# Kernel optimization log

Hardware: AMD Instinct MI355X
Metric: run time of the kernel (lower is better)

The kernel has to match this reference:

```python
import jax, jax.numpy as jnp
import numpy as np

EMBED = 1024
HEADS = 16
HEAD_DIM = EMBED // HEADS
HIDDEN = 4 * EMBED
EPS = 1e-5


def setup_inputs() -> dict:
    key = jax.random.key(0)
    ks = jax.random.split(key, 9)
    s = lambda fan_in: 1.0 / np.sqrt(fan_in)
    inp = {
        "x": jax.random.normal(ks[0], (2, 2048, EMBED), dtype=jnp.float32),
        "ln1_w": jnp.ones((EMBED,), jnp.float32),
        "ln1_b": jnp.zeros((EMBED,), jnp.float32),
        "ln2_w": jnp.ones((EMBED,), jnp.float32),
        "ln2_b": jnp.zeros((EMBED,), jnp.float32),
        "qkv_w": jax.random.uniform(ks[1], (EMBED, 3 * EMBED), jnp.float32, -s(EMBED), s(EMBED)),
        "qkv_b": jax.random.uniform(ks[2], (3 * EMBED,), jnp.float32, -s(EMBED), s(EMBED)),
        "proj_w": jax.random.uniform(ks[3], (EMBED, EMBED), jnp.float32, -s(EMBED), s(EMBED)),
        "proj_b": jax.random.uniform(ks[4], (EMBED,), jnp.float32, -s(EMBED), s(EMBED)),
        "fc1_w": jax.random.uniform(ks[5], (EMBED, HIDDEN), jnp.float32, -s(EMBED), s(EMBED)),
        "fc1_b": jax.random.uniform(ks[6], (HIDDEN,), jnp.float32, -s(EMBED), s(EMBED)),
        "fc2_w": jax.random.uniform(ks[7], (HIDDEN, EMBED), jnp.float32, -s(HIDDEN), s(HIDDEN)),
        "fc2_b": jax.random.uniform(ks[8], (EMBED,), jnp.float32, -s(HIDDEN), s(HIDDEN)),
    }
    return inp


def _layernorm(x, w, b):
    mu = jnp.mean(x, axis=-1, keepdims=True)
    var = jnp.mean(jnp.square(x - mu), axis=-1, keepdims=True)
    return (x - mu) * jax.lax.rsqrt(var + EPS) * w + b


def _attn(x, qkv_w, qkv_b, proj_w, proj_b):
    B, N, C = x.shape
    qkv = x @ qkv_w + qkv_b                      # [B,N,3C]
    qkv = qkv.reshape(B, N, 3, HEADS, HEAD_DIM)
    q, k, v = qkv[:, :, 0], qkv[:, :, 1], qkv[:, :, 2]   # [B,N,H,D]
    scale = HEAD_DIM ** -0.5
    scores = jnp.einsum("bqhd,bkhd->bhqk", q, k) * scale  # [B,H,N,N]
    attn = jax.nn.softmax(scores, axis=-1)
    out = jnp.einsum("bhqk,bkhd->bqhd", attn, v).reshape(B, N, C)
    return out @ proj_w + proj_b


def _mlp(x, fc1_w, fc1_b, fc2_w, fc2_b):
    h = jax.nn.gelu(x @ fc1_w + fc1_b, approximate=False)
    return h @ fc2_w + fc2_b


def reference(x, ln1_w, ln1_b, ln2_w, ln2_b, qkv_w, qkv_b, proj_w, proj_b,
              fc1_w, fc1_b, fc2_w, fc2_b):
    # pre-norm transformer block (eval mode: dropout/drop_path are identity)
    x = x + _attn(_layernorm(x, ln1_w, ln1_b), qkv_w, qkv_b, proj_w, proj_b)
    x = x + _mlp(_layernorm(x, ln2_w, ln2_b), fc1_w, fc1_b, fc2_w, fc2_b)
    return x
```

## Files before the change

### kernel.cpp

```cpp
#include <hip/hip_runtime.h>
#include <hip/hip_bf16.h>

#define SEQ    2048
#define BATCH  2
#define MTOK   4096
#define EMBED  1024
#define HEADS  16
#define HDIM   64
#define QKV3   3072
#define FFN    4096

typedef __attribute__((ext_vector_type(8))) short bf16x8;
typedef __attribute__((ext_vector_type(4))) float f32x4;
typedef __attribute__((ext_vector_type(16))) float f32x16;

static __device__ __forceinline__ unsigned short f2bf(float f) {
  union { float f; unsigned u; } x; x.f = f;
  unsigned r = x.u + 0x7FFFu + ((x.u >> 16) & 1u);
  return (unsigned short)(r >> 16);
}
static __device__ __forceinline__ float bf2f(unsigned short u) {
  union { unsigned u; float f; } x; x.u = ((unsigned)u) << 16; return x.f;
}
static __device__ __forceinline__ unsigned pk2bf(float a, float b) {
#if __has_builtin(__builtin_amdgcn_cvt_pk_bf16_f32)
  typedef __attribute__((ext_vector_type(2))) __bf16 bf16x2_t;
  union { bf16x2_t v; unsigned u; } x;
  x.v = __builtin_amdgcn_cvt_pk_bf16_f32(a, b);
  return x.u;
#else
  return ((unsigned)f2bf(a)) | (((unsigned)f2bf(b)) << 16);
#endif
}
static __device__ __forceinline__ float fexp2(float x) {
#if __has_builtin(__builtin_amdgcn_exp2f)
  return __builtin_amdgcn_exp2f(x);
#else
  return exp2f(x);
#endif
}
static __device__ __forceinline__ float frcp(float x) {
#if __has_builtin(__builtin_amdgcn_rcpf)
  return __builtin_amdgcn_rcpf(x);
#else
  return 1.0f / x;
#endif
}
static __device__ __forceinline__ float fgelu(float v) {
  float t = v * v;
  float z = v * __builtin_fmaf(-0.1029456f, t, -2.3022650687f);
  return v * frcp(1.0f + fexp2(z));
}

static __device__ __forceinline__ void halfswap(unsigned a, unsigned b, int hi,
                                                unsigned& lo_out, unsigned& hi_out) {
#if __has_builtin(__builtin_amdgcn_permlane32_swap)
  typedef __attribute__((ext_vector_type(2))) unsigned uint2v;
  uint2v r = __builtin_amdgcn_permlane32_swap(a, b, false, false);
  lo_out = r[0];
  hi_out = r[1];
#else
  unsigned as = (unsigned)__shfl_xor((int)a, 32);
  unsigned bs = (unsigned)__shfl_xor((int)b, 32);
  lo_out = hi ? bs : a;
  hi_out = hi ? b : as;
#endif
}

static __device__ __forceinline__ void gload16(const unsigned short* g, unsigned short* l) {
  __builtin_amdgcn_global_load_lds((const __attribute__((address_space(1))) void*)g,
                                   (__attribute__((address_space(3))) void*)l, 16, 0, 0);
}

#define MEMFENCE asm volatile("" ::: "memory")

struct TD { const float* W; unsigned short* T; int K, N, ntx, base; };
struct TD4 { TD d[4]; };

__global__ void transpose_all(TD4 td) {
  __shared__ float t[32][33];
  int bid = blockIdx.x;
  int i = 0;
  if (bid >= td.d[1].base) i = 1;
  if (bid >= td.d[2].base) i = 2;
  if (bid >= td.d[3].base) i = 3;
  const TD& D = td.d[i];
  int local = bid - D.base;
  int n0 = (local % D.ntx) * 32, k0 = (local / D.ntx) * 32;
  int tx = threadIdx.x, ty = threadIdx.y;
#pragma unroll
  for (int j = 0; j < 32; j += 8)
    t[ty + j][tx] = D.W[(size_t)(k0 + ty + j) * D.N + n0 + tx];
  __syncthreads();
#pragma unroll
  for (int j = 0; j < 32; j += 8)
    D.T[(size_t)(n0 + ty + j) * D.K + k0 + tx] = f2bf(t[tx][ty + j]);
}

__global__ __launch_bounds__(256) void ln_kernel(const float* __restrict__ in,
                                                 const float* __restrict__ w,
                                                 const float* __restrict__ b,
                                                 unsigned short* __restrict__ out) {
  __shared__ float sh[4];
  int row = blockIdx.x, tid = threadIdx.x;
  const float4 v = ((const float4*)(in + (size_t)row * EMBED))[tid];
  float s = v.x + v.y + v.z + v.w;
#pragma unroll
  for (int off = 32; off; off >>= 1) s += __shfl_xor(s, off);
  if ((tid & 63) == 0) sh[tid >> 6] = s;
  __syncthreads();
  float mean = (sh[0] + sh[1] + sh[2] + sh[3]) * (1.0f / EMBED);
  __syncthreads();
  float dx = v.x - mean, dy = v.y - mean, dz = v.z - mean, dw = v.w - mean;
  float q = dx * dx + dy * dy + dz * dz + dw * dw;
#pragma unroll
  for (int off = 32; off; off >>= 1) q += __shfl_xor(q, off);
  if ((tid & 63) == 0) sh[tid >> 6] = q;
  __syncthreads();
  float var = (sh[0] + sh[1] + sh[2] + sh[3]) * (1.0f / EMBED);
  float rs = rsqrtf(var + 1e-5f);
  const float4 wv = ((const float4*)w)[tid];
  const float4 bv = ((const float4*)b)[tid];
  ushort4 o;
  o.x = f2bf(dx * rs * wv.x + bv.x);
  o.y = f2bf(dy * rs * wv.y + bv.y);
  o.z = f2bf(dz * rs * wv.z + bv.z);
  o.w = f2bf(dw * rs * wv.w + bv.w);
  ((ushort4*)(out + (size_t)row * EMBED))[tid] = o;
}

template <int ACT, int OUTBF, int VSPLIT>
__global__ __launch_bounds__(256) void gemmBig(const unsigned short* __restrict__ A,
                                               const unsigned short* __restrict__ Wt,
                                               const float* __restrict__ bias,
                                               unsigned short* __restrict__ outB,
                                               float* __restrict__ outF,
                                               unsigned short* __restrict__ vT,
                                               int M, int N, int K, int nblk) {
  __shared__ __align__(16) unsigned short As[128 * 64];
  __shared__ __align__(16) unsigned short Bs[128 * 64];
  const int tid = threadIdx.x;
  const int wave = tid >> 6, lane = tid & 63;
  const int quad = lane >> 4, ml = lane & 15;
  const int wr = wave >> 1, wc = wave & 1;
  const int m0 = (blockIdx.x / nblk) * 128;
  const int n0 = (blockIdx.x % nblk) * 128;
  const int srow = lane >> 3;
  const int schunk = (lane & 7) ^ (srow & 7);
  const unsigned short* Ag = A + (size_t)(m0 + wave * 32 + srow) * K + schunk * 8;
  const unsigned short* Bg = Wt + (size_t)(n0 + wave * 32 + srow) * K + schunk * 8;
  unsigned short* AsW = &As[wave * 2048];
  unsigned short* BsW = &Bs[wave * 2048];
  f32x4 acc[4][4];
#pragma unroll
  for (int i = 0; i < 4; i++)
#pragma unroll
    for (int j = 0; j < 4; j++) acc[i][j] = (f32x4){0.f, 0.f, 0.f, 0.f};
  for (int k0 = 0; k0 < K; k0 += 64) {
    __syncthreads();
#pragma unroll
    for (int t = 0; t < 4; t++) {
      gload16(Ag + (size_t)(8 * t) * K, AsW + 512 * t);
      gload16(Bg + (size_t)(8 * t) * K, BsW + 512 * t);
    }
    Ag += 64; Bg += 64;
    __syncthreads();
#pragma unroll
    for (int kh = 0; kh < 2; kh++) {
      const int ch = ((kh * 4 + quad) ^ (ml & 7)) * 8;
      bf16x8 af[4], bfr[4];
#pragma unroll
      for (int mt = 0; mt < 4; mt++)
        af[mt] = *(const bf16x8*)&As[(wr * 64 + mt * 16 + ml) * 64 + ch];
#pragma unroll
      for (int nt = 0; nt < 4; nt++)
        bfr[nt] = *(const bf16x8*)&Bs[(wc * 64 + nt * 16 + ml) * 64 + ch];
#pragma unroll
      for (int mt = 0; mt < 4; mt++)
#pragma unroll
        for (int nt = 0; nt < 4; nt++)
          acc[mt][nt] = __builtin_amdgcn_mfma_f32_16x16x32_bf16(af[mt], bfr[nt], acc[mt][nt], 0, 0, 0);
    }
  }
#pragma unroll
  for (int mt = 0; mt < 4; mt++)
#pragma unroll
    for (int nt = 0; nt < 4; nt++) {
      const int col0 = n0 + wc * 64 + nt * 16;
      const int row0 = m0 + wr * 64 + mt * 16;
      if (VSPLIT && col0 >= 2 * EMBED) {
        const int b = row0 >> 11, tok0 = row0 & (SEQ - 1);
        const int h = (col0 - 2 * EMBED) >> 6;
        const int dl = ((col0 - 2 * EMBED) & 63) + ml;
        float bia = bias[col0 + ml];
        ushort4 o;
        o.x = f2bf(acc[mt][nt][0] + bia);
        o.y = f2bf(acc[mt][nt][1] + bia);
        o.z = f2bf(acc[mt][nt][2] + bia);
        o.w = f2bf(acc[mt][nt][3] + bia);
        *(ushort4*)(vT + (size_t)((b * 16 + h) * 64 + dl) * SEQ + tok0 + quad * 4) = o;
      } else {
#pragma unroll
        for (int r = 0; r < 4; r++) {
          int row = row0 + quad * 4 + r;
          int col = col0 + ml;
          float v = acc[mt][nt][r] + bias[col];
          if (ACT) v = fgelu(v);
          if (OUTBF)
            outB[(size_t)row * N + col] = f2bf(v);
          else
            outF[(size_t)row * N + col] = v;
        }
      }
    }
}

template <int ACT, int VSPLIT>
__global__ __launch_bounds__(512, 2) void gemm256(const unsigned short* __restrict__ A,
                                                  const unsigned short* __restrict__ Wt,
                                                  const float* __restrict__ bias,
                                                  unsigned short* __restrict__ outB,
                                                  unsigned short* __restrict__ vT,
                                                  int M, int N, int K, int nblk) {
  __shared__ __align__(16) unsigned short As[2][256 * 64];
  __shared__ __align__(16) unsigned short Bs[2][256 * 64];
  const int tid = threadIdx.x;
  const int wave = tid >> 6, lane = tid & 63;
  const int quad = lane >> 4, ml = lane & 15;
  const int wr = wave >> 2, wc = wave & 3;
  const int m0 = (blockIdx.x / nblk) * 256;
  const int n0 = (blockIdx.x % nblk) * 256;
  const int srow = lane >> 3;
  const int schunk = (lane & 7) ^ (srow & 7);
  const unsigned short* Ag = A  + (size_t)(m0 + wave * 32 + srow) * K + schunk * 8;
  const unsigned short* Bg = Wt + (size_t)(n0 + wave * 32 + srow) * K + schunk * 8;
  f32x4 acc[8][4];
#pragma unroll
  for (int i = 0; i < 8; i++)
#pragma unroll
    for (int j = 0; j < 4; j++) acc[i][j] = (f32x4){0.f, 0.f, 0.f, 0.f};

#pragma unroll
  for (int g = 0; g < 4; g++) {
    gload16(Ag + (size_t)(g * 8) * K, &As[0][(wave * 32 + g * 8) * 64]);
    gload16(Bg + (size_t)(g * 8) * K, &Bs[0][(wave * 32 + g * 8) * 64]);
  }

  const int nit = K >> 7;
  for (int it = 0; it < nit; ++it) {
#pragma unroll
    for (int half = 0; half < 2; ++half) {
      const int rs = half;
      const int ss = half ^ 1;
      const int kst = 2 * it + 1 + half;
      const bool doStage = (kst < 2 * nit);
      const unsigned short* Asl = &As[rs][0];
      const unsigned short* Bsl = &Bs[rs][0];
      bf16x8 bfr[4][2];
#pragma unroll
      for (int ph = 0; ph < 4; ++ph) {
        bf16x8 af[2][2];
        if (ph > 0) {
#pragma unroll
          for (int mt2 = 0; mt2 < 2; ++mt2)
#pragma unroll
            for (int kk = 0; kk < 2; ++kk)
              af[mt2][kk] = *(const bf16x8*)&Asl[(wr * 128 + (ph * 2 + mt2) * 16 + ml) * 64 +
                                                ((kk * 4 + quad) ^ (ml & 7)) * 8];
        }
        if (doStage) {
          if (ph < 2) {
            gload16(Ag + (size_t)((ph * 2) * 8) * K + kst * 64,
                    &As[ss][(wave * 32 + (ph * 2) * 8) * 64]);
            gload16(Ag + (size_t)((ph * 2 + 1) * 8) * K + kst * 64,
                    &As[ss][(wave * 32 + (ph * 2 + 1) * 8) * 64]);
          } else {
            gload16(Bg + (size_t)(((ph - 2) * 2) * 8) * K + kst * 64,
                    &Bs[ss][(wave * 32 + ((ph - 2) * 2) * 8) * 64]);
            gload16(Bg + (size_t)(((ph - 2) * 2 + 1) * 8) * K + kst * 64,
                    &Bs[ss][(wave * 32 + ((ph - 2) * 2 + 1) * 8) * 64]);
          }
        }
        if (ph == 0) {
          if (doStage) { asm volatile("s_waitcnt vmcnt(2)" ::: "memory"); }
          else         { asm volatile("s_waitcnt vmcnt(0)" ::: "memory"); }
          MEMFENCE; __builtin_amdgcn_s_barrier(); MEMFENCE;
#pragma unroll
          for (int nt = 0; nt < 4; ++nt)
#pragma unroll
            for (int kk = 0; kk < 2; ++kk)
              bfr[nt][kk] = *(const bf16x8*)&Bsl[(wc * 64 + nt * 16 + ml) * 64 +
                                                ((kk * 4 + quad) ^ (ml & 7)) * 8];
#pragma unroll
          for (int mt2 = 0; mt2 < 2; ++mt2)
#pragma unroll
            for (int kk = 0; kk < 2; ++kk)
              af[mt2][kk] = *(const bf16x8*)&Asl[(wr * 128 + mt2 * 16 + ml) * 64 +
                                                ((kk * 4 + quad) ^ (ml & 7)) * 8];
        } else {
          MEMFENCE; __builtin_amdgcn_s_barrier(); MEMFENCE;
        }
        __builtin_amdgcn_s_setprio(1);
#pragma unroll
        for (int mt2 = 0; mt2 < 2; ++mt2)
#pragma unroll
          for (int nt = 0; nt < 4; ++nt)
#pragma unroll
            for (int kk = 0; kk < 2; ++kk)
              acc[ph * 2 + mt2][nt] = __builtin_amdgcn_mfma_f32_16x16x32_bf16(
                  af[mt2][kk], bfr[nt][kk], acc[ph * 2 + mt2][nt], 0, 0, 0);
        __builtin_amdgcn_s_setprio(0);
        MEMFENCE; __builtin_amdgcn_s_barrier(); MEMFENCE;
      }
    }
  }
#pragma unroll
  for (int mt = 0; mt < 8; ++mt)
#pragma unroll
    for (int nt = 0; nt < 4; ++nt) {
      const int col0 = n0 + wc * 64 + nt * 16;
      const int row0 = m0 + wr * 128 + mt * 16;
      if (VSPLIT && col0 >= 2 * EMBED) {
        const int b = row0 >> 11, tok0 = row0 & (SEQ - 1);
        const int h = (col0 - 2 * EMBED) >> 6;
        const int dl = ((col0 - 2 * EMBED) & 63) + ml;
        float bia = bias[col0 + ml];
        ushort4 o;
        o.x = f2bf(acc[mt][nt][0] + bia);
        o.y = f2bf(acc[mt][nt][1] + bia);
        o.z = f2bf(acc[mt][nt][2] + bia);
        o.w = f2bf(acc[mt][nt][3] + bia);
        *(ushort4*)(vT + (size_t)((b * 16 + h) * 64 + dl) * SEQ + tok0 + quad * 4) = o;
      } else {
#pragma unroll
        for (int r = 0; r < 4; ++r) {
          int row = row0 + quad * 4 + r;
          int col = col0 + ml;
          float v = acc[mt][nt][r] + bias[col];
          if (ACT) v = fgelu(v);
          outB[(size_t)row * N + col] = f2bf(v);
        }
      }
    }
}

template <int RES, int OUTBF>
__global__ __launch_bounds__(256) void gemm64k(const unsigned short* __restrict__ A,
                                               const unsigned short* __restrict__ Wt,
                                               const float* __restrict__ bias,
                                               const float* __restrict__ res,
                                               unsigned short* __restrict__ outB,
                                               float* __restrict__ outF,
                                               int M, int N, int K, int nblk) {
  __shared__ __align__(16) unsigned short As[3][128 * 64];
  __shared__ __align__(16) unsigned short Bs[3][64 * 64];
  const int tid = threadIdx.x;
  const int wave = tid >> 6, lane = tid & 63;
  const int quad = lane >> 4, ml = lane & 15;
  const int wr = wave >> 1, wc = wave & 1;
  const int xcd = blockIdx.x & 7, idx = blockIdx.x >> 3;
  const int mPerXcd = (gridDim.x >> 3) / nblk;
  const int m0 = (xcd * mPerXcd + idx / nblk) * 128;
  const int n0 = (idx % nblk) * 64;
  const int srow = lane >> 3;
  const int schunk = (lane & 7) ^ (srow & 7);
  const unsigned short* Ag = A + (size_t)(m0 + wave * 32 + srow) * K + schunk * 8;
  const unsigned short* Bg = Wt + (size_t)(n0 + wave * 16 + srow) * K + schunk * 8;
  f32x4 acc[4][2];
#pragma unroll
  for (int i = 0; i < 4; i++) { acc[i][0] = (f32x4){0.f,0.f,0.f,0.f}; acc[i][1] = acc[i][0]; }

#pragma unroll
  for (int p = 0; p < 2; ++p) {
    unsigned short* AsW = &As[p][wave * 2048];
    unsigned short* BsW = &Bs[p][wave * 1024];
    gload16(Ag, AsW);
    gload16(Ag + (size_t)8 * K,  AsW + 512);
    gload16(Ag + (size_t)16 * K, AsW + 1024);
    gload16(Ag + (size_t)24 * K, AsW + 1536);
    gload16(Bg, BsW);
    gload16(Bg + (size_t)8 * K,  BsW + 512);
    Ag += 64; Bg += 64;
  }

  const int nk = K >> 6;
  int ss = 2;
  for (int kk = 0; kk < nk; ++kk) {
    if (kk + 2 < nk) {
      unsigned short* AsW = &As[ss][wave * 2048];
      unsigned short* BsW = &Bs[ss][wave * 1024];
      gload16(Ag, AsW);
      gload16(Ag + (size_t)8 * K,  AsW + 512);
      gload16(Ag + (size_t)16 * K, AsW + 1024);
      gload16(Ag + (size_t)24 * K, AsW + 1536);
      gload16(Bg, BsW);
      gload16(Bg + (size_t)8 * K,  BsW + 512);
      Ag += 64; Bg += 64;
      asm volatile("s_waitcnt vmcnt(12)" ::: "memory");
    } else if (kk + 1 < nk) {
      asm volatile("s_waitcnt vmcnt(6)" ::: "memory");
    } else {
      asm volatile("s_waitcnt vmcnt(0)" ::: "memory");
    }
    MEMFENCE; __builtin_amdgcn_s_barrier(); MEMFENCE;
    const int cs = kk - 3 * ((kk * 0x5556) >> 16);
    const unsigned short* Asl = &As[cs][0];
    const unsigned short* Bsl = &Bs[cs][0];
#pragma unroll
    for (int kh = 0; kh < 2; kh++) {
      const int ch = ((kh * 4 + quad) ^ (ml & 7)) * 8;
      bf16x8 af[4], bfr[2];
#pragma unroll
      for (int mt = 0; mt < 4; mt++)
        af[mt] = *(const bf16x8*)&Asl[(wr * 64 + mt * 16 + ml) * 64 + ch];
#pragma unroll
      for (int nt = 0; nt < 2; nt++)
        bfr[nt] = *(const bf16x8*)&Bsl[(wc * 32 + nt * 16 + ml) * 64 + ch];
#pragma unroll
      for (int mt = 0; mt < 4; mt++)
#pragma unroll
        for (int nt = 0; nt < 2; nt++)
          acc[mt][nt] = __builtin_amdgcn_mfma_f32_16x16x32_bf16(af[mt], bfr[nt], acc[mt][nt], 0, 0, 0);
    }
    MEMFENCE; __builtin_amdgcn_s_barrier(); MEMFENCE;
    ss = (ss == 2) ? 0 : ss + 1;
  }
#pragma unroll
  for (int mt = 0; mt < 4; mt++)
#pragma unroll
    for (int nt = 0; nt < 2; nt++)
#pragma unroll
      for (int r = 0; r < 4; r++) {
        int row = m0 + wr * 64 + mt * 16 + quad * 4 + r;
        int col = n0 + wc * 32 + nt * 16 + ml;
        float v = acc[mt][nt][r] + bias[col];
        if (RES) v += res[(size_t)row * N + col];
        if (OUTBF)
          outB[(size_t)row * N + col] = f2bf(v);
        else
          outF[(size_t)row * N + col] = v;
      }
}

__global__ __launch_bounds__(256, 4) void attn_kernel(const unsigned short* __restrict__ qkv,
                                                      const unsigned short* __restrict__ vT,
                                                      unsigned short* __restrict__ attn) {
  __shared__ __align__(16) unsigned short Ks[2][64 * 64];
  __shared__ __align__(16) unsigned short Vs[2][64 * 64];
  const int tid = threadIdx.x, wave = tid >> 6, lane = tid & 63;
  const int l31 = lane & 31, hi = lane >> 5;
  const int qs = wave & 1, kh = wave >> 1;
  const int bh = blockIdx.x, b = bh >> 4, h = bh & 15;
  const int q0w = blockIdx.y * 64 + qs * 32;
  const float qscale = 0.18033688011112042f;
  const int sw = l31 & 7;

  const unsigned short* qrow = qkv + (size_t)(b * SEQ + q0w + l31) * QKV3 + h * HDIM;
  bf16x8 bq[4];
#pragma unroll
  for (int s = 0; s < 4; s++) {
    bq[s] = *(const bf16x8*)(qrow + s * 16 + hi * 8);
#pragma unroll
    for (int j = 0; j < 8; j++)
      bq[s][j] = (short)f2bf(bf2f((unsigned short)bq[s][j]) * qscale);
  }
  bf16x8 ones;
#pragma unroll
  for (int j = 0; j < 8; j++) ones[j] = (short)0x3F80;

  f32x16 zz;
#pragma unroll
  for (int i = 0; i < 16; i++) zz[i] = 0.f;
  f32x16 O0 = zz, O1 = zz, lsum = zz;

  const int skey = lane >> 3;
  const int schunk8 = ((lane & 7) ^ (skey & 7)) * 8;
  const unsigned short* kbase =
      qkv + (size_t)(b * SEQ + wave * 16 + skey) * QKV3 + EMBED + h * HDIM + schunk8;
  const unsigned short* vbase =
      vT + (size_t)(bh * 64 + wave * 16 + skey) * SEQ + schunk8;

  gload16(kbase, &Ks[0][wave * 1024]);
  gload16(kbase + (size_t)8 * QKV3, &Ks[0][wave * 1024] + 512);
  gload16(vbase, &Vs[0][wave * 1024]);
  gload16(vbase + (size_t)8 * SEQ, &Vs[0][wave * 1024] + 512);
  __syncthreads();

  const int krow0 = kh * 32;
  for (int kti = 0; kti < SEQ / 64; ++kti) {
    const int cur = kti & 1;
    if (kti + 1 < SEQ / 64) {
      const int kt = (kti + 1) * 64;
      unsigned short* kd = &Ks[cur ^ 1][wave * 1024];
      unsigned short* vd = &Vs[cur ^ 1][wave * 1024];
      gload16(kbase + (size_t)kt * QKV3, kd);
      gload16(kbase + (size_t)(kt + 8) * QKV3, kd + 512);
      gload16(vbase + kt, vd);
      gload16(vbase + kt + (size_t)8 * SEQ, vd + 512);
    }
    const unsigned short* Kc = &Ks[cur][0];
    const unsigned short* Vc = &Vs[cur][0];

    f32x16 St = zz;
#pragma unroll
    for (int s = 0; s < 4; s++) {
      bf16x8 ak = *(const bf16x8*)&Kc[(krow0 + l31) * 64 + ((2 * s + hi) ^ sw) * 8];
      St = __builtin_amdgcn_mfma_f32_32x32x16_bf16(ak, bq[s], St, 0, 0, 0);
    }

    unsigned W0[4], W1[4];
#pragma unroll
    for (int g = 0; g < 4; g++) {
      W0[g] = pk2bf(fexp2(St[4 * g]), fexp2(St[4 * g + 1]));
      W1[g] = pk2bf(fexp2(St[4 * g + 2]), fexp2(St[4 * g + 3]));
    }

    bf16x8 pa[2];
#pragma unroll
    for (int ks = 0; ks < 2; ks++) {
      const int g0 = 2 * ks, g1 = g0 + 1;
      unsigned w0, w1, w2, w3;
      halfswap(W0[g0], W0[g1], hi, w0, w2);
      halfswap(W1[g0], W1[g1], hi, w1, w3);
      union { unsigned u[4]; bf16x8 v; } pw;
      pw.u[0] = w0; pw.u[1] = w1; pw.u[2] = w2; pw.u[3] = w3;
      pa[ks] = pw.v;
    }

    __builtin_amdgcn_s_setprio(1);
    lsum = __builtin_amdgcn_mfma_f32_32x32x16_bf16(pa[0], ones, lsum, 0, 0, 0);
    lsum = __builtin_amdgcn_mfma_f32_32x32x16_bf16(pa[1], ones, lsum, 0, 0, 0);
#pragma unroll
    for (int ks = 0; ks < 2; ks++) {
      const int ch = kh * 4 + ks * 2 + hi;
      bf16x8 bv0 = *(const bf16x8*)&Vc[l31 * 64 + (ch ^ sw) * 8];
      bf16x8 bv1 = *(const bf16x8*)&Vc[(32 + l31) * 64 + (ch ^ sw) * 8];
      O0 = __builtin_amdgcn_mfma_f32_32x32x16_bf16(pa[ks], bv0, O0, 0, 0, 0);
      O1 = __builtin_amdgcn_mfma_f32_32x32x16_bf16(pa[ks], bv1, O1, 0, 0, 0);
    }
    __builtin_amdgcn_s_setprio(0);
    __syncthreads();
  }

  if (kh == 1) {
    float* sc = qs ? (float*)&Vs[0][0] : (float*)&Ks[0][0];
#pragma unroll
    for (int r = 0; r < 16; r++) {
      sc[lane * 49 + r]      = lsum[r];
      sc[lane * 49 + 16 + r] = O0[r];
      sc[lane * 49 + 32 + r] = O1[r];
    }
  }
  __syncthreads();
  if (kh == 0) {
    const float* sc = qs ? (const float*)&Vs[0][0] : (const float*)&Ks[0][0];
#pragma unroll
    for (int r = 0; r < 16; r++) {
      lsum[r] += sc[lane * 49 + r];
      O0[r]   += sc[lane * 49 + 16 + r];
      O1[r]   += sc[lane * 49 + 32 + r];
    }
#pragma unroll
    for (int r = 0; r < 16; r++) {
      const int qr = (r & 3) + 8 * (r >> 2) + 4 * hi;
      float inv = 1.0f / lsum[r];
      size_t g = (size_t)(b * SEQ + q0w + qr) * EMBED + h * HDIM + l31;
      attn[g]      = f2bf(O0[r] * inv);
      attn[g + 32] = f2bf(O1[r] * inv);
    }
  }
}

extern "C" void kernel_launch(void* const* d_in, const int* in_sizes, int n_in,
                              void* d_out, int out_size, void* d_ws, size_t ws_size,
                              hipStream_t stream) {
  const float* x      = (const float*)d_in[0];
  const float* ln1_w  = (const float*)d_in[1];
  const float* ln1_b  = (const float*)d_in[2];
  const float* ln2_w  = (const float*)d_in[3];
  const float* ln2_b  = (const float*)d_in[4];
  const float* qkv_w  = (const float*)d_in[5];
  const float* qkv_b  = (const float*)d_in[6];
  const float* proj_w = (const float*)d_in[7];
  const float* proj_b = (const float*)d_in[8];
  const float* fc1_w  = (const float*)d_in[9];
  const float* fc1_b  = (const float*)d_in[10];
  const float* fc2_w  = (const float*)d_in[11];
  const float* fc2_b  = (const float*)d_in[12];
  float* out = (float*)d_out;
  char* wsb = (char*)d_ws;
  unsigned short* lnbuf  = (unsigned short*)(wsb + 0);
  unsigned short* qkvb   = (unsigned short*)(wsb + 8388608);
  unsigned short* attnb  = (unsigned short*)(wsb + 33554432);
  unsigned short* vTb    = (unsigned short*)(wsb + 41943040);
  unsigned short* actb   = (unsigned short*)(wsb + 33554432);
  float*          h1     = (float*)(wsb + 67108864);
  unsigned short* qkvWt  = (unsigned short*)(wsb + 83886080);
  unsigned short* projWt = (unsigned short*)(wsb + 90177536);
  unsigned short* fc1Wt  = (unsigned short*)(wsb + 92274688);
  unsigned short* fc2Wt  = (unsigned short*)(wsb + 100663296);

  TD4 td;
  td.d[0] = {qkv_w,  qkvWt,  1024, 3072,  96, 0};
  td.d[1] = {proj_w, projWt, 1024, 1024,  32, 3072};
  td.d[2] = {fc1_w,  fc1Wt,  1024, 4096, 128, 4096};
  td.d[3] = {fc2_w,  fc2Wt,  4096, 1024,  32, 8192};
  transpose_all<<<12288, dim3(32, 8), 0, stream>>>(td);

  ln_kernel<<<MTOK, 256, 0, stream>>>(x, ln1_w, ln1_b, lnbuf);
  gemmBig<0, 1, 1><<<768, 256, 0, stream>>>(
      lnbuf, qkvWt, qkv_b, qkvb, nullptr, vTb, MTOK, QKV3, EMBED, 24);
  attn_kernel<<<dim3(32, 32), 256, 0, stream>>>(qkvb, vTb, attnb);
  gemm64k<1, 0><<<512, 256, 0, stream>>>(
      attnb, projWt, proj_b, x, nullptr, h1, MTOK, EMBED, EMBED, 16);
  ln_kernel<<<MTOK, 256, 0, stream>>>(h1, ln2_w, ln2_b, lnbuf);
  gemm256<1, 0><<<256, 512, 0, stream>>>(
      lnbuf, fc1Wt, fc1_b, actb, nullptr, MTOK, FFN, EMBED, 16);
  gemm64k<1, 0><<<512, 256, 0, stream>>>(
      actb, fc2Wt, fc2_b, h1, nullptr, out, MTOK, EMBED, FFN, 16);
}
```

Baseline: 337.9 us.

## Double attention block to 8 waves with 128-key tiles and four-way key split

The attention kernel moves from 256 to 512 threads. Each block now stages 128-key K/V tiles per iteration with a new 16-way XOR swizzle for the V tile, so half as many loop iterations and barriers are needed. The key dimension is split across four wave groups instead of two, and partial softmax sums and outputs are combined in a two-stage shared-memory reduction. Shared memory per block doubles and extra barriers are added at the end, which may limit occupancy under the 512x4 launch bound.

Result: no change. 340.0 us (+0.6%).

```diff
diff --git a/kernel.cpp b/kernel.cpp
--- a/kernel.cpp
+++ b/kernel.cpp
@@ -442,11 +442,11 @@
       }
 }
 
-__global__ __launch_bounds__(256, 4) void attn_kernel(const unsigned short* __restrict__ qkv,
+__global__ __launch_bounds__(512, 4) void attn_kernel(const unsigned short* __restrict__ qkv,
                                                       const unsigned short* __restrict__ vT,
                                                       unsigned short* __restrict__ attn) {
-  __shared__ __align__(16) unsigned short Ks[2][64 * 64];
-  __shared__ __align__(16) unsigned short Vs[2][64 * 64];
+  __shared__ __align__(16) unsigned short Ks[2][128 * 64];
+  __shared__ __align__(16) unsigned short Vs[2][64 * 128];
   const int tid = threadIdx.x, wave = tid >> 6, lane = tid & 63;
   const int l31 = lane & 31, hi = lane >> 5;
   const int qs = wave & 1, kh = wave >> 1;
@@ -477,26 +477,28 @@
   const int schunk8 = ((lane & 7) ^ (skey & 7)) * 8;
   const unsigned short* kbase =
       qkv + (size_t)(b * SEQ + wave * 16 + skey) * QKV3 + EMBED + h * HDIM + schunk8;
-  const unsigned short* vbase =
-      vT + (size_t)(bh * 64 + wave * 16 + skey) * SEQ + schunk8;
+  const int vr0 = wave * 8 + (lane >> 4);
+  const int vr1 = vr0 + 4;
+  const unsigned short* vbase0 =
+      vT + (size_t)(bh * 64 + vr0) * SEQ + (((lane & 15) ^ (vr0 & 15)) * 8);
+  const unsigned short* vbase1 =
+      vT + (size_t)(bh * 64 + vr1) * SEQ + (((lane & 15) ^ (vr1 & 15)) * 8);
 
   gload16(kbase, &Ks[0][wave * 1024]);
   gload16(kbase + (size_t)8 * QKV3, &Ks[0][wave * 1024] + 512);
-  gload16(vbase, &Vs[0][wave * 1024]);
-  gload16(vbase + (size_t)8 * SEQ, &Vs[0][wave * 1024] + 512);
+  gload16(vbase0, &Vs[0][wave * 1024]);
+  gload16(vbase1, &Vs[0][wave * 1024 + 512]);
   __syncthreads();
 
   const int krow0 = kh * 32;
-  for (int kti = 0; kti < SEQ / 64; ++kti) {
+  for (int kti = 0; kti < SEQ / 128; ++kti) {
     const int cur = kti & 1;
-    if (kti + 1 < SEQ / 64) {
-      const int kt = (kti + 1) * 64;
-      unsigned short* kd = &Ks[cur ^ 1][wave * 1024];
-      unsigned short* vd = &Vs[cur ^ 1][wave * 1024];
-      gload16(kbase + (size_t)kt * QKV3, kd);
-      gload16(kbase + (size_t)(kt + 8) * QKV3, kd + 512);
-      gload16(vbase + kt, vd);
-      gload16(vbase + kt + (size_t)8 * SEQ, vd + 512);
+    if (kti + 1 < SEQ / 128) {
+      const int kt = (kti + 1) * 128;
+      gload16(kbase + (size_t)kt * QKV3, &Ks[cur ^ 1][wave * 1024]);
+      gload16(kbase + (size_t)(kt + 8) * QKV3, &Ks[cur ^ 1][wave * 1024] + 512);
+      gload16(vbase0 + kt, &Vs[cur ^ 1][wave * 1024]);
+      gload16(vbase1 + kt, &Vs[cur ^ 1][wave * 1024 + 512]);
     }
     const unsigned short* Kc = &Ks[cur][0];
     const unsigned short* Vc = &Vs[cur][0];
@@ -533,8 +535,8 @@
 #pragma unroll
     for (int ks = 0; ks < 2; ks++) {
       const int ch = kh * 4 + ks * 2 + hi;
-      bf16x8 bv0 = *(const bf16x8*)&Vc[l31 * 64 + (ch ^ sw) * 8];
-      bf16x8 bv1 = *(const bf16x8*)&Vc[(32 + l31) * 64 + (ch ^ sw) * 8];
+      bf16x8 bv0 = *(const bf16x8*)&Vc[l31 * 128 + ((ch ^ (l31 & 15))) * 8];
+      bf16x8 bv1 = *(const bf16x8*)&Vc[(32 + l31) * 128 + ((ch ^ (l31 & 15))) * 8];
       O0 = __builtin_amdgcn_mfma_f32_32x32x16_bf16(pa[ks], bv0, O0, 0, 0, 0);
       O1 = __builtin_amdgcn_mfma_f32_32x32x16_bf16(pa[ks], bv1, O1, 0, 0, 0);
     }
@@ -542,8 +544,10 @@
     __syncthreads();
   }
 
-  if (kh == 1) {
-    float* sc = qs ? (float*)&Vs[0][0] : (float*)&Ks[0][0];
+  float* A2 = qs ? (float*)&Vs[0][0] : (float*)&Ks[0][0];
+  float* A3 = qs ? (float*)&Vs[1][0] : (float*)&Ks[1][0];
+  if (kh == 2 || kh == 3) {
+    float* sc = (kh == 2) ? A2 : A3;
 #pragma unroll
     for (int r = 0; r < 16; r++) {
       sc[lane * 49 + r]      = lsum[r];
@@ -552,13 +556,31 @@
     }
   }
   __syncthreads();
-  if (kh == 0) {
-    const float* sc = qs ? (const float*)&Vs[0][0] : (const float*)&Ks[0][0];
+  if (kh == 0 || kh == 1) {
+    const float* sc = (kh == 0) ? A2 : A3;
 #pragma unroll
     for (int r = 0; r < 16; r++) {
       lsum[r] += sc[lane * 49 + r];
       O0[r]   += sc[lane * 49 + 16 + r];
       O1[r]   += sc[lane * 49 + 32 + r];
+    }
+  }
+  __syncthreads();
+  if (kh == 1) {
+#pragma unroll
+    for (int r = 0; r < 16; r++) {
+      A2[lane * 49 + r]      = lsum[r];
+      A2[lane * 49 + 16 + r] = O0[r];
+      A2[lane * 49 + 32 + r] = O1[r];
+    }
+  }
+  __syncthreads();
+  if (kh == 0) {
+#pragma unroll
+    for (int r = 0; r < 16; r++) {
+      lsum[r] += A2[lane * 49 + r];
+      O0[r]   += A2[lane * 49 + 16 + r];
+      O1[r]   += A2[lane * 49 + 32 + r];
     }
 #pragma unroll
     for (int r = 0; r < 16; r++) {
@@ -610,7 +632,7 @@
   ln_kernel<<<MTOK, 256, 0, stream>>>(x, ln1_w, ln1_b, lnbuf);
   gemmBig<0, 1, 1><<<768, 256, 0, stream>>>(
       lnbuf, qkvWt, qkv_b, qkvb, nullptr, vTb, MTOK, QKV3, EMBED, 24);
-  attn_kernel<<<dim3(32, 32), 256, 0, stream>>>(qkvb, vTb, attnb);
+  attn_kernel<<<dim3(32, 32), 512, 0, stream>>>(qkvb, vTb, attnb);
   gemm64k<1, 0><<<512, 256, 0, stream>>>(
       attnb, projWt, proj_b, x, nullptr, h1, MTOK, EMBED, EMBED, 16);
   ln_kernel<<<MTOK, 256, 0, stream>>>(h1, ln2_w, ln2_b, lnbuf);
```

## Split-K the fc2 GEMM into two halves with a separate reduce kernel

Applied to the files above, without the earlier changes.

The fc2 GEMM (K=4096) now launches 1024 blocks, each computing half of the K range and writing fp32 partial sums to a workspace buffer. A new reduce kernel then adds the two partials, the bias and the residual. The aim is to double the block count so the long-K GEMM fills more CUs. In exchange it adds 32 MB of partial-sum traffic and an extra kernel launch.

After: 346.4 us. 1.03x slower.

```diff
diff --git a/kernel.cpp b/kernel.cpp
--- a/kernel.cpp
+++ b/kernel.cpp
@@ -344,28 +344,31 @@
     }
 }
 
-template <int RES, int OUTBF>
+template <int RES, int OUTBF, int WRPART>
 __global__ __launch_bounds__(256) void gemm64k(const unsigned short* __restrict__ A,
                                                const unsigned short* __restrict__ Wt,
                                                const float* __restrict__ bias,
                                                const float* __restrict__ res,
                                                unsigned short* __restrict__ outB,
                                                float* __restrict__ outF,
-                                               int M, int N, int K, int nblk) {
+                                               int M, int N, int K, int kext,
+                                               int nblk, int nxb) {
   __shared__ __align__(16) unsigned short As[3][128 * 64];
   __shared__ __align__(16) unsigned short Bs[3][64 * 64];
   const int tid = threadIdx.x;
   const int wave = tid >> 6, lane = tid & 63;
   const int quad = lane >> 4, ml = lane & 15;
   const int wr = wave >> 1, wc = wave & 1;
-  const int xcd = blockIdx.x & 7, idx = blockIdx.x >> 3;
-  const int mPerXcd = (gridDim.x >> 3) / nblk;
+  const int ks = (blockIdx.x >= nxb) ? 1 : 0;
+  const int bx = blockIdx.x - ks * nxb;
+  const int xcd = bx & 7, idx = bx >> 3;
+  const int mPerXcd = (nxb >> 3) / nblk;
   const int m0 = (xcd * mPerXcd + idx / nblk) * 128;
   const int n0 = (idx % nblk) * 64;
   const int srow = lane >> 3;
   const int schunk = (lane & 7) ^ (srow & 7);
-  const unsigned short* Ag = A + (size_t)(m0 + wave * 32 + srow) * K + schunk * 8;
-  const unsigned short* Bg = Wt + (size_t)(n0 + wave * 16 + srow) * K + schunk * 8;
+  const unsigned short* Ag = A + (size_t)(m0 + wave * 32 + srow) * K + ks * kext + schunk * 8;
+  const unsigned short* Bg = Wt + (size_t)(n0 + wave * 16 + srow) * K + ks * kext + schunk * 8;
   f32x4 acc[4][2];
 #pragma unroll
   for (int i = 0; i < 4; i++) { acc[i][0] = (f32x4){0.f,0.f,0.f,0.f}; acc[i][1] = acc[i][0]; }
@@ -383,7 +386,7 @@
     Ag += 64; Bg += 64;
   }
 
-  const int nk = K >> 6;
+  const int nk = kext >> 6;
   int ss = 2;
   for (int kk = 0; kk < nk; ++kk) {
     if (kk + 2 < nk) {
@@ -433,13 +436,36 @@
       for (int r = 0; r < 4; r++) {
         int row = m0 + wr * 64 + mt * 16 + quad * 4 + r;
         int col = n0 + wc * 32 + nt * 16 + ml;
-        float v = acc[mt][nt][r] + bias[col];
+        float v = acc[mt][nt][r];
+        if (!WRPART) v += bias[col];
         if (RES) v += res[(size_t)row * N + col];
-        if (OUTBF)
+        if (WRPART)
+          outF[(size_t)ks * M * N + (size_t)row * N + col] = v;
+        else if (OUTBF)
           outB[(size_t)row * N + col] = f2bf(v);
         else
           outF[(size_t)row * N + col] = v;
       }
+}
+
+__global__ __launch_bounds__(256) void fc2_reduce(const float* __restrict__ p,
+                                                  const float* __restrict__ res,
+                                                  const float* __restrict__ bias,
+                                                  float* __restrict__ out) {
+#pragma unroll
+  for (int k = 0; k < 2; ++k) {
+    const size_t i4 = (size_t)blockIdx.x * 512 + k * 256 + threadIdx.x;
+    const float4 a = ((const float4*)p)[i4];
+    const float4 b = ((const float4*)p)[i4 + (size_t)MTOK * EMBED / 4];
+    const float4 r = ((const float4*)res)[i4];
+    const float4 bb = ((const float4*)bias)[i4 & 255];
+    float4 o;
+    o.x = a.x + b.x + r.x + bb.x;
+    o.y = a.y + b.y + r.y + bb.y;
+    o.z = a.z + b.z + r.z + bb.z;
+    o.w = a.w + b.w + r.w + bb.w;
+    ((float4*)out)[i4] = o;
+  }
 }
 
 __global__ __launch_bounds__(256, 4) void attn_kernel(const unsigned short* __restrict__ qkv,
@@ -595,6 +621,7 @@
   unsigned short* vTb    = (unsigned short*)(wsb + 41943040);
   unsigned short* actb   = (unsigned short*)(wsb + 33554432);
   float*          h1     = (float*)(wsb + 67108864);
+  float*          fc2p   = (float*)(wsb + 0);
   unsigned short* qkvWt  = (unsigned short*)(wsb + 83886080);
   unsigned short* projWt = (unsigned short*)(wsb + 90177536);
   unsigned short* fc1Wt  = (unsigned short*)(wsb + 92274688);
@@ -611,11 +638,12 @@
   gemmBig<0, 1, 1><<<768, 256, 0, stream>>>(
       lnbuf, qkvWt, qkv_b, qkvb, nullptr, vTb, MTOK, QKV3, EMBED, 24);
   attn_kernel<<<dim3(32, 32), 256, 0, stream>>>(qkvb, vTb, attnb);
-  gemm64k<1, 0><<<512, 256, 0, stream>>>(
-      attnb, projWt, proj_b, x, nullptr, h1, MTOK, EMBED, EMBED, 16);
+  gemm64k<1, 0, 0><<<512, 256, 0, stream>>>(
+      attnb, projWt, proj_b, x, nullptr, h1, MTOK, EMBED, EMBED, EMBED, 16, 512);
   ln_kernel<<<MTOK, 256, 0, stream>>>(h1, ln2_w, ln2_b, lnbuf);
   gemm256<1, 0><<<256, 512, 0, stream>>>(
       lnbuf, fc1Wt, fc1_b, actb, nullptr, MTOK, FFN, EMBED, 16);
-  gemm64k<1, 0><<<512, 256, 0, stream>>>(
-      actb, fc2Wt, fc2_b, h1, nullptr, out, MTOK, EMBED, FFN, 16);
-}
+  gemm64k<0, 0, 1><<<1024, 256, 0, stream>>>(
+      actb, fc2Wt, nullptr, nullptr, nullptr, fc2p, MTOK, EMBED, FFN, 2048, 16, 512);
+  fc2_reduce<<<2048, 256, 0, stream>>>(fc2p, h1, fc2_b, out);
+}
```

## Software-pipeline attention loop: overlap next QK^T with current PV using triple-buffered V

Applied to the files above, without the earlier changes.

Restructures the attention inner loop so the QK^T MFMAs for tile k run in the same iteration as the exp/PV work for tile k-1. This exposes independent MFMA work to hide the exp and LDS latency. V tiles move to a triple buffer so the previous tile's V stays resident while the next one loads, and a prologue and epilogue handle the pipeline edges. It adds LDS usage and register pressure from keeping two score tiles live, which may hurt occupancy under launch_bounds(256,4).

New measurement: 341.1 us. About the same (+1.0%).

```diff
diff --git a/kernel.cpp b/kernel.cpp
--- a/kernel.cpp
+++ b/kernel.cpp
@@ -446,7 +446,7 @@
                                                       const unsigned short* __restrict__ vT,
                                                       unsigned short* __restrict__ attn) {
   __shared__ __align__(16) unsigned short Ks[2][64 * 64];
-  __shared__ __align__(16) unsigned short Vs[2][64 * 64];
+  __shared__ __align__(16) unsigned short Vs[3][64 * 64];
   const int tid = threadIdx.x, wave = tid >> 6, lane = tid & 63;
   const int l31 = lane & 31, hi = lane >> 5;
   const int qs = wave & 1, kh = wave >> 1;
@@ -479,42 +479,47 @@
       qkv + (size_t)(b * SEQ + wave * 16 + skey) * QKV3 + EMBED + h * HDIM + schunk8;
   const unsigned short* vbase =
       vT + (size_t)(bh * 64 + wave * 16 + skey) * SEQ + schunk8;
+  const int krow0 = kh * 32;
 
   gload16(kbase, &Ks[0][wave * 1024]);
   gload16(kbase + (size_t)8 * QKV3, &Ks[0][wave * 1024] + 512);
   gload16(vbase, &Vs[0][wave * 1024]);
   gload16(vbase + (size_t)8 * SEQ, &Vs[0][wave * 1024] + 512);
+  gload16(kbase + (size_t)64 * QKV3, &Ks[1][wave * 1024]);
+  gload16(kbase + (size_t)72 * QKV3, &Ks[1][wave * 1024] + 512);
+  gload16(vbase + 64, &Vs[1][wave * 1024]);
+  gload16(vbase + 64 + (size_t)8 * SEQ, &Vs[1][wave * 1024] + 512);
   __syncthreads();
 
-  const int krow0 = kh * 32;
-  for (int kti = 0; kti < SEQ / 64; ++kti) {
-    const int cur = kti & 1;
+  f32x16 Stp = zz;
+#pragma unroll
+  for (int s = 0; s < 4; s++) {
+    bf16x8 ak = *(const bf16x8*)&Ks[0][(krow0 + l31) * 64 + ((2 * s + hi) ^ sw) * 8];
+    Stp = __builtin_amdgcn_mfma_f32_32x32x16_bf16(ak, bq[s], Stp, 0, 0, 0);
+  }
+
+  int vprev = 0, vnext = 2;
+  for (int kti = 1; kti < SEQ / 64; ++kti) {
+    const int kc = kti & 1;
     if (kti + 1 < SEQ / 64) {
       const int kt = (kti + 1) * 64;
-      unsigned short* kd = &Ks[cur ^ 1][wave * 1024];
-      unsigned short* vd = &Vs[cur ^ 1][wave * 1024];
-      gload16(kbase + (size_t)kt * QKV3, kd);
-      gload16(kbase + (size_t)(kt + 8) * QKV3, kd + 512);
-      gload16(vbase + kt, vd);
-      gload16(vbase + kt + (size_t)8 * SEQ, vd + 512);
-    }
-    const unsigned short* Kc = &Ks[cur][0];
-    const unsigned short* Vc = &Vs[cur][0];
-
-    f32x16 St = zz;
+      gload16(kbase + (size_t)kt * QKV3, &Ks[kc ^ 1][wave * 1024]);
+      gload16(kbase + (size_t)(kt + 8) * QKV3, &Ks[kc ^ 1][wave * 1024] + 512);
+      gload16(vbase + kt, &Vs[vnext][wave * 1024]);
+      gload16(vbase + kt + (size_t)8 * SEQ, &Vs[vnext][wave * 1024] + 512);
+    }
+    f32x16 Stc = zz;
 #pragma unroll
     for (int s = 0; s < 4; s++) {
-      bf16x8 ak = *(const bf16x8*)&Kc[(krow0 + l31) * 64 + ((2 * s + hi) ^ sw) * 8];
-      St = __builtin_amdgcn_mfma_f32_32x32x16_bf16(ak, bq[s], St, 0, 0, 0);
-    }
-
+      bf16x8 ak = *(const bf16x8*)&Ks[kc][(krow0 + l31) * 64 + ((2 * s + hi) ^ sw) * 8];
+      Stc = __builtin_amdgcn_mfma_f32_32x32x16_bf16(ak, bq[s], Stc, 0, 0, 0);
+    }
     unsigned W0[4], W1[4];
 #pragma unroll
     for (int g = 0; g < 4; g++) {
-      W0[g] = pk2bf(fexp2(St[4 * g]), fexp2(St[4 * g + 1]));
-      W1[g] = pk2bf(fexp2(St[4 * g + 2]), fexp2(St[4 * g + 3]));
-    }
-
+      W0[g] = pk2bf(fexp2(Stp[4 * g]), fexp2(Stp[4 * g + 1]));
+      W1[g] = pk2bf(fexp2(Stp[4 * g + 2]), fexp2(Stp[4 * g + 3]));
+    }
     bf16x8 pa[2];
 #pragma unroll
     for (int ks = 0; ks < 2; ks++) {
@@ -526,21 +531,53 @@
       pw.u[0] = w0; pw.u[1] = w1; pw.u[2] = w2; pw.u[3] = w3;
       pa[ks] = pw.v;
     }
-
     __builtin_amdgcn_s_setprio(1);
     lsum = __builtin_amdgcn_mfma_f32_32x32x16_bf16(pa[0], ones, lsum, 0, 0, 0);
     lsum = __builtin_amdgcn_mfma_f32_32x32x16_bf16(pa[1], ones, lsum, 0, 0, 0);
 #pragma unroll
     for (int ks = 0; ks < 2; ks++) {
       const int ch = kh * 4 + ks * 2 + hi;
-      bf16x8 bv0 = *(const bf16x8*)&Vc[l31 * 64 + (ch ^ sw) * 8];
-      bf16x8 bv1 = *(const bf16x8*)&Vc[(32 + l31) * 64 + (ch ^ sw) * 8];
+      bf16x8 bv0 = *(const bf16x8*)&Vs[vprev][l31 * 64 + (ch ^ sw) * 8];
+      bf16x8 bv1 = *(const bf16x8*)&Vs[vprev][(32 + l31) * 64 + (ch ^ sw) * 8];
       O0 = __builtin_amdgcn_mfma_f32_32x32x16_bf16(pa[ks], bv0, O0, 0, 0, 0);
       O1 = __builtin_amdgcn_mfma_f32_32x32x16_bf16(pa[ks], bv1, O1, 0, 0, 0);
     }
     __builtin_amdgcn_s_setprio(0);
     __syncthreads();
-  }
+    Stp = Stc;
+    vprev = (vprev == 2) ? 0 : vprev + 1;
+    vnext = (vnext == 2) ? 0 : vnext + 1;
+  }
+  {
+    unsigned W0[4], W1[4];
+#pragma unroll
+    for (int g = 0; g < 4; g++) {
+      W0[g] = pk2bf(fexp2(Stp[4 * g]), fexp2(Stp[4 * g + 1]));
+      W1[g] = pk2bf(fexp2(Stp[4 * g + 2]), fexp2(Stp[4 * g + 3]));
+    }
+    bf16x8 pa[2];
+#pragma unroll
+    for (int ks = 0; ks < 2; ks++) {
+      const int g0 = 2 * ks, g1 = g0 + 1;
+      unsigned w0, w1, w2, w3;
+      halfswap(W0[g0], W0[g1], hi, w0, w2);
+      halfswap(W1[g0], W1[g1], hi, w1, w3);
+      union { unsigned u[4]; bf16x8 v; } pw;
+      pw.u[0] = w0; pw.u[1] = w1; pw.u[2] = w2; pw.u[3] = w3;
+      pa[ks] = pw.v;
+    }
+    lsum = __builtin_amdgcn_mfma_f32_32x32x16_bf16(pa[0], ones, lsum, 0, 0, 0);
+    lsum = __builtin_amdgcn_mfma_f32_32x32x16_bf16(pa[1], ones, lsum, 0, 0, 0);
+#pragma unroll
+    for (int ks = 0; ks < 2; ks++) {
+      const int ch = kh * 4 + ks * 2 + hi;
+      bf16x8 bv0 = *(const bf16x8*)&Vs[vprev][l31 * 64 + (ch ^ sw) * 8];
+      bf16x8 bv1 = *(const bf16x8*)&Vs[vprev][(32 + l31) * 64 + (ch ^ sw) * 8];
+      O0 = __builtin_amdgcn_mfma_f32_32x32x16_bf16(pa[ks], bv0, O0, 0, 0, 0);
+      O1 = __builtin_amdgcn_mfma_f32_32x32x16_bf16(pa[ks], bv1, O1, 0, 0, 0);
+    }
+  }
+  __syncthreads();
 
   if (kh == 1) {
     float* sc = qs ? (float*)&Vs[0][0] : (float*)&Ks[0][0];
```
